# Kernel tuning notes

Measured on AMD Instinct MI355X. Metric: run time of the kernel, lower is better.

## Reference

```python
import jax, jax.numpy as jnp
import numpy as np

EPS = 1e-12

def l2norm(v, axis):
    return v / jnp.maximum(jnp.linalg.norm(v, axis=axis, keepdims=True), EPS)

def setup_inputs() -> dict:
    key = jax.random.key(0)
    k1, k2, k3, k4 = jax.random.split(key, 4)
    N, C, S, K = 16, 128, 16384, 64
    return {
        "x": jax.random.normal(k1, (N, C, S), dtype=jnp.float32),
        "fc_w": jax.random.normal(k2, (K, C), dtype=jnp.float32),
        "fc_b": jax.random.normal(k3, (K,), dtype=jnp.float32),
        "centroids": jax.random.uniform(k4, (K, C), dtype=jnp.float32),
    }

def reference(x, fc_w, fc_b, centroids):
    # x: [N, C, S]; fc_w: [K, C]; centroids: [K, C]
    x = l2norm(x, axis=1)  # descriptor-wise L2 normalize over channels
    # 1x1 conv (per-position linear) -> soft assignment over clusters
    logits = jnp.einsum('ncs,kc->nks', x, fc_w) + fc_b[None, :, None]
    soft = jax.nn.softmax(logits, axis=1)  # [N, K, S]
    # vlad[n,k,c] = sum_s soft[n,k,s] * (x[n,c,s] - centroids[k,c])
    # matmul decomposition avoids materializing [N,K,C,S]
    a_sum = soft.sum(axis=-1)  # [N, K]
    vlad = jnp.einsum('nks,ncs->nkc', soft, x) - a_sum[:, :, None] * centroids[None]
    vlad = l2norm(vlad, axis=2)            # intra-normalization
    vlad = vlad.reshape(vlad.shape[0], -1)  # [N, K*C]
    vlad = l2norm(vlad, axis=1)            # final L2 normalize
    return vlad
```

## Files before the change

### kernel.cpp

```cpp
#include <hip/hip_runtime.h>
#include <hip/hip_fp16.h>

#define N_ 16
#define C_ 128
#define S_ 16384
#define K_ 64

typedef __attribute__((ext_vector_type(4))) float f32x4;
typedef __attribute__((ext_vector_type(8))) _Float16 f16x8;
typedef __attribute__((ext_vector_type(4))) _Float16 f16x4;

#define SWZ_S(s) ((((s) ^ ((s) >> 3)) & 7) << 3)

__global__ __launch_bounds__(256, 2) void fused_kernel(
    const float* __restrict__ x, const float* __restrict__ fc_w,
    const float* __restrict__ fc_b, float* __restrict__ vlad_part,
    float* __restrict__ a_part)
{
    __shared__ _Float16 xT[64 * 128];
    __shared__ _Float16 xC[2][128 * 64];
    __shared__ _Float16 sst[64 * 64];
    __shared__ float rns[2][64];

    const int tid = threadIdx.x;
    const int n = blockIdx.x >> 5;
    const int chunk = blockIdx.x & 31;
    const int lane = tid & 63, w = tid >> 6;
    const int lr = lane & 15, g = lane >> 4;
    const int fsw = (lr & 7) << 3;

    f16x8 wfrag[4][4];
#pragma unroll
    for (int nt = 0; nt < 4; ++nt)
#pragma unroll
        for (int kt = 0; kt < 4; ++kt) {
            const float* wp = fc_w + (nt * 16 + lr) * C_ + kt * 32 + g * 8;
            float4 wa = *(const float4*)wp;
            float4 wb = *(const float4*)(wp + 4);
            f16x8 f;
            f[0] = (_Float16)wa.x; f[1] = (_Float16)wa.y;
            f[2] = (_Float16)wa.z; f[3] = (_Float16)wa.w;
            f[4] = (_Float16)wb.x; f[5] = (_Float16)wb.y;
            f[6] = (_Float16)wb.z; f[7] = (_Float16)wb.w;
            wfrag[nt][kt] = f;
        }
    if (tid < 128) (&rns[0][0])[tid] = 0.f;

    float bias[4];
#pragma unroll
    for (int nt = 0; nt < 4; ++nt) bias[nt] = fc_b[nt * 16 + lr];
    float a_acc[4] = {0.f, 0.f, 0.f, 0.f};
    f32x4 vacc[8];
#pragma unroll
    for (int nt = 0; nt < 8; ++nt) vacc[nt] = (f32x4){0.f, 0.f, 0.f, 0.f};
    f32x4 accp[4];

    const float* xb = x + (size_t)n * C_ * S_;
    const int s4 = tid & 15;
    int cqv[2];
#pragma unroll
    for (int i = 0; i < 2; ++i) cqv[i] = i * 16 + (tid >> 4);

    float4 pre[2][4];
#pragma unroll
    for (int i = 0; i < 2; ++i)
#pragma unroll
        for (int cc = 0; cc < 4; ++cc)
            pre[i][cc] = *(const float4*)(xb + (size_t)(cqv[i] * 4 + cc) * S_ +
                                          chunk * 512 + s4 * 4);

    auto softmax_emit = [&](int pit) {
        float rnl[4], ai[4];
#pragma unroll
        for (int r = 0; r < 4; ++r)
            rnl[r] = 1.0f / fmaxf(sqrtf(rns[pit][w * 16 + g * 4 + r]), 1e-12f);
        if (lane < 16) rns[pit][w * 16 + lane] = 0.f;
#pragma unroll
        for (int nt = 0; nt < 4; ++nt)
#pragma unroll
            for (int r = 0; r < 4; ++r)
                accp[nt][r] = __expf(accp[nt][r] * rnl[r] + bias[nt]);
#pragma unroll
        for (int r = 0; r < 4; ++r) {
            float sum = (accp[0][r] + accp[1][r]) + (accp[2][r] + accp[3][r]);
            sum += __shfl_xor(sum, 1);
            sum += __shfl_xor(sum, 2);
            sum += __shfl_xor(sum, 4);
            sum += __shfl_xor(sum, 8);
            float bi = 1.0f / sum;
            ai[r] = bi * rnl[r];
#pragma unroll
            for (int nt = 0; nt < 4; ++nt) a_acc[nt] += accp[nt][r] * bi;
        }
#pragma unroll
        for (int nt = 0; nt < 4; ++nt) {
            int k = nt * 16 + lr;
            int sloc = w * 16 + g * 4;
            f16x4 p = {(_Float16)(accp[nt][0] * ai[0]), (_Float16)(accp[nt][1] * ai[1]),
                       (_Float16)(accp[nt][2] * ai[2]), (_Float16)(accp[nt][3] * ai[3])};
            *(f16x4*)&sst[k * 64 + (sloc ^ ((k & 7) << 3))] = p;
        }
    };

#pragma unroll 1
    for (int it = 0; it < 8; ++it) {
        const int b = it & 1;
        __syncthreads();

        float part[4] = {0.f, 0.f, 0.f, 0.f};
#pragma unroll
        for (int i = 0; i < 2; ++i) {
            int cq = cqv[i];
#pragma unroll
            for (int jj = 0; jj < 4; ++jj) {
                float v0 = (&pre[i][0].x)[jj], v1 = (&pre[i][1].x)[jj],
                      v2 = (&pre[i][2].x)[jj], v3 = (&pre[i][3].x)[jj];
                part[jj] += v0 * v0 + v1 * v1 + v2 * v2 + v3 * v3;
                f16x4 p = {(_Float16)v0, (_Float16)v1, (_Float16)v2, (_Float16)v3};
                int s = s4 * 4 + jj;
                *(f16x4*)&xT[s * 128 + ((cq * 4) ^ SWZ_S(s))] = p;
            }
#pragma unroll
            for (int cc = 0; cc < 4; ++cc) {
                int c = cq * 4 + cc;
                f16x4 q = {(_Float16)pre[i][cc].x, (_Float16)pre[i][cc].y,
                           (_Float16)pre[i][cc].z, (_Float16)pre[i][cc].w};
                *(f16x4*)&xC[b][c * 64 + ((s4 * 4) ^ ((c & 7) << 3))] = q;
            }
        }
#pragma unroll
        for (int jj = 0; jj < 4; ++jj) {
            part[jj] += __shfl_xor(part[jj], 16);
            part[jj] += __shfl_xor(part[jj], 32);
        }
        if (g == 0) {
#pragma unroll
            for (int jj = 0; jj < 4; ++jj)
                atomicAdd(&rns[it & 1][lr * 4 + jj], part[jj]);
        }
        if (it > 0) softmax_emit((it - 1) & 1);
        if (it < 7) {
            const float* xb2 = xb + chunk * 512 + (it + 1) * 64;
#pragma unroll
            for (int i = 0; i < 2; ++i)
#pragma unroll
                for (int cc = 0; cc < 4; ++cc)
                    pre[i][cc] = *(const float4*)(xb2 + (size_t)(cqv[i] * 4 + cc) * S_ + s4 * 4);
        }
        __syncthreads();

#pragma unroll
        for (int nt = 0; nt < 4; ++nt) accp[nt] = (f32x4){0.f, 0.f, 0.f, 0.f};
        __builtin_amdgcn_s_setprio(1);
#pragma unroll
        for (int kt = 0; kt < 4; ++kt) {
            const int co = kt * 32 + g * 8;
            const int sa = w * 16 + lr;
            f16x8 af = *(const f16x8*)&xT[sa * 128 + (co ^ SWZ_S(sa))];
#pragma unroll
            for (int nt = 0; nt < 4; ++nt)
                accp[nt] = __builtin_amdgcn_mfma_f32_16x16x32_f16(af, wfrag[nt][kt], accp[nt], 0, 0, 0);
        }
        if (it > 0) {
            const _Float16* xcp = xC[b ^ 1];
#pragma unroll
            for (int kt = 0; kt < 2; ++kt) {
                const int so = kt * 32 + g * 8;
                f16x8 pa = *(const f16x8*)&sst[(w * 16 + lr) * 64 + (so ^ fsw)];
#pragma unroll
                for (int nt = 0; nt < 8; ++nt) {
                    f16x8 xv = *(const f16x8*)&xcp[(nt * 16 + lr) * 64 + (so ^ fsw)];
                    vacc[nt] = __builtin_amdgcn_mfma_f32_16x16x32_f16(pa, xv, vacc[nt], 0, 0, 0);
                }
            }
        }
        __builtin_amdgcn_s_setprio(0);
    }

    __syncthreads();
    softmax_emit(1);
    __syncthreads();
    {
        const _Float16* xcp = xC[1];
#pragma unroll
        for (int kt = 0; kt < 2; ++kt) {
            const int so = kt * 32 + g * 8;
            f16x8 pa = *(const f16x8*)&sst[(w * 16 + lr) * 64 + (so ^ fsw)];
#pragma unroll
            for (int nt = 0; nt < 8; ++nt) {
                f16x8 xv = *(const f16x8*)&xcp[(nt * 16 + lr) * 64 + (so ^ fsw)];
                vacc[nt] = __builtin_amdgcn_mfma_f32_16x16x32_f16(pa, xv, vacc[nt], 0, 0, 0);
            }
        }
    }

    float* vp = vlad_part + (size_t)blockIdx.x * (K_ * C_) + (w * 16) * C_;
#pragma unroll
    for (int nt = 0; nt < 8; ++nt)
#pragma unroll
        for (int r = 0; r < 4; ++r)
            vp[(g * 4 + r) * C_ + nt * 16 + lr] = vacc[nt][r];
#pragma unroll
    for (int nt = 0; nt < 4; ++nt) {
        a_acc[nt] += __shfl_xor(a_acc[nt], 16);
        a_acc[nt] += __shfl_xor(a_acc[nt], 32);
    }
    if (lane < 16) {
#pragma unroll
        for (int nt = 0; nt < 4; ++nt)
            a_part[blockIdx.x * 256 + w * 64 + nt * 16 + lr] = a_acc[nt];
    }
}

__global__ __launch_bounds__(256) void reduce_kernel(
    const float* __restrict__ vlad_part, float* __restrict__ vlad_sum)
{
    const int n = blockIdx.x >> 5, g8 = blockIdx.x & 31;
    const int e = g8 * 256 + threadIdx.x;
    const float* p = vlad_part + (size_t)(n * 32) * (K_ * C_) + e;
    float acc = 0.f;
#pragma unroll
    for (int ch = 0; ch < 32; ++ch) acc += p[(size_t)ch * (K_ * C_)];
    vlad_sum[n * (K_ * C_) + e] = acc;
}

__global__ __launch_bounds__(1024) void finalize_kernel(
    const float* __restrict__ vlad_sum, const float* __restrict__ a_part,
    const float* __restrict__ centroids, float* __restrict__ out)
{
    __shared__ float red[16];
    const int n = blockIdx.x;
    const int t = threadIdx.x;
    const int k = t >> 4, q = t & 15;

    float av = 0.f;
#pragma unroll
    for (int cc = 0; cc < 2; ++cc) {
        int ch = q * 2 + cc;
        const float* ap = a_part + (size_t)(n * 32 + ch) * 256 + k;
#pragma unroll
        for (int ww = 0; ww < 4; ++ww) av += ap[ww * 64];
    }
    av += __shfl_xor(av, 1);
    av += __shfl_xor(av, 2);
    av += __shfl_xor(av, 4);
    av += __shfl_xor(av, 8);

    const float* vp = vlad_sum + (size_t)n * (K_ * C_) + k * C_;
    const float* cp = centroids + k * C_;
    float v[8];
    float ssq = 0.f;
#pragma unroll
    for (int jj = 0; jj < 8; ++jj) {
        int c = q + 16 * jj;
        float val = vp[c] - av * cp[c];
        v[jj] = val;
        ssq += val * val;
    }
    ssq += __shfl_xor(ssq, 1);
    ssq += __shfl_xor(ssq, 2);
    ssq += __shfl_xor(ssq, 4);
    ssq += __shfl_xor(ssq, 8);
    const float inv1 = 1.0f / fmaxf(sqrtf(ssq), 1e-12f);

    float gp = (q == 0) ? ssq * inv1 * inv1 : 0.f;
#pragma unroll
    for (int off = 1; off < 64; off <<= 1) gp += __shfl_xor(gp, off);
    if ((t & 63) == 0) red[t >> 6] = gp;
    __syncthreads();
    float G = 0.f;
#pragma unroll
    for (int i = 0; i < 16; ++i) G += red[i];
    const float ginv = 1.0f / fmaxf(sqrtf(G), 1e-12f);

    float* op = out + (size_t)n * (K_ * C_) + k * C_;
#pragma unroll
    for (int jj = 0; jj < 8; ++jj) op[q + 16 * jj] = v[jj] * inv1 * ginv;
}

extern "C" void kernel_launch(void* const* d_in, const int* in_sizes, int n_in,
                              void* d_out, int out_size, void* d_ws, size_t ws_size,
                              hipStream_t stream) {
    const float* x     = (const float*)d_in[0];
    const float* fc_w  = (const float*)d_in[1];
    const float* fc_b  = (const float*)d_in[2];
    const float* cent  = (const float*)d_in[3];
    float* out = (float*)d_out;

    char* ws = (char*)d_ws;
    float* vlad_part = (float*)ws;
    float* a_part    = (float*)(ws + (size_t)512 * K_ * C_ * 4);
    float* vlad_sum  = (float*)(ws + (size_t)512 * K_ * C_ * 4 + 512 * 1024);

    fused_kernel<<<N_ * 32, 256, 0, stream>>>(x, fc_w, fc_b, vlad_part, a_part);
    reduce_kernel<<<N_ * 32, 256, 0, stream>>>(vlad_part, vlad_sum);
    finalize_kernel<<<N_, 1024, 0, stream>>>(vlad_sum, a_part, cent, out);
}
```

Before: 53.85 us.

## Use FP8 MFMA for VLAD aggregation and rebalance grid to 48 chunks per batch

The soft-assignment and x tiles used for the VLAD aggregation matmul are now stored in LDS as FP8, and that matmul runs on fp8×fp8 MFMA. The soft weights are scaled by 256 to keep them in FP8 range, and the scale is undone on output. The grid grows from 512 to 768 blocks, 48 per batch, each handling 5 or 6 tiles of 64 positions, so work spreads more evenly across CUs. This halves LDS traffic for that stage and raises occupancy, at the cost of FP8 accuracy loss, a larger partial buffer, and more partials to reduce.

New measurement: 65.83 us. 22.2% more time.

```diff
diff --git a/kernel.cpp b/kernel.cpp
--- a/kernel.cpp
+++ b/kernel.cpp
@@ -11,6 +11,14 @@
 typedef __attribute__((ext_vector_type(4))) _Float16 f16x4;
 
 #define SWZ_S(s) ((((s) ^ ((s) >> 3)) & 7) << 3)
+#define SWZ8(r) (((r) & 7) << 3)
+
+static __device__ __forceinline__ unsigned int pack_fp8x4(float a, float b,
+                                                          float c, float d) {
+    int v = __builtin_amdgcn_cvt_pk_fp8_f32(a, b, 0, false);
+    v = __builtin_amdgcn_cvt_pk_fp8_f32(c, d, v, true);
+    return (unsigned int)v;
+}
 
 __global__ __launch_bounds__(256, 2) void fused_kernel(
     const float* __restrict__ x, const float* __restrict__ fc_w,
@@ -18,16 +26,19 @@
     float* __restrict__ a_part)
 {
     __shared__ _Float16 xT[64 * 128];
-    __shared__ _Float16 xC[2][128 * 64];
-    __shared__ _Float16 sst[64 * 64];
+    __shared__ __align__(16) unsigned char xC8[2][128 * 64];
+    __shared__ __align__(16) unsigned char sst8[64 * 64];
     __shared__ float rns[2][64];
 
     const int tid = threadIdx.x;
-    const int n = blockIdx.x >> 5;
-    const int chunk = blockIdx.x & 31;
     const int lane = tid & 63, w = tid >> 6;
     const int lr = lane & 15, g = lane >> 4;
-    const int fsw = (lr & 7) << 3;
+    const int fsw = SWZ8(lr);
+
+    const int b = blockIdx.x;
+    const int n = b / 48, j = b % 48;
+    const int lo  = (j < 16) ? j * 6 : 96 + (j - 16) * 5;
+    const int cnt = (j < 16) ? 6 : 5;
 
     f16x8 wfrag[4][4];
 #pragma unroll
@@ -67,7 +78,7 @@
 #pragma unroll
         for (int cc = 0; cc < 4; ++cc)
             pre[i][cc] = *(const float4*)(xb + (size_t)(cqv[i] * 4 + cc) * S_ +
-                                          chunk * 512 + s4 * 4);
+                                          lo * 64 + s4 * 4);
 
     auto softmax_emit = [&](int pit) {
         float rnl[4], ai[4];
@@ -88,7 +99,7 @@
             sum += __shfl_xor(sum, 4);
             sum += __shfl_xor(sum, 8);
             float bi = 1.0f / sum;
-            ai[r] = bi * rnl[r];
+            ai[r] = bi * rnl[r] * 256.0f;
 #pragma unroll
             for (int nt = 0; nt < 4; ++nt) a_acc[nt] += accp[nt][r] * bi;
         }
@@ -96,15 +107,15 @@
         for (int nt = 0; nt < 4; ++nt) {
             int k = nt * 16 + lr;
             int sloc = w * 16 + g * 4;
-            f16x4 p = {(_Float16)(accp[nt][0] * ai[0]), (_Float16)(accp[nt][1] * ai[1]),
-                       (_Float16)(accp[nt][2] * ai[2]), (_Float16)(accp[nt][3] * ai[3])};
-            *(f16x4*)&sst[k * 64 + (sloc ^ ((k & 7) << 3))] = p;
+            unsigned int pk = pack_fp8x4(accp[nt][0] * ai[0], accp[nt][1] * ai[1],
+                                         accp[nt][2] * ai[2], accp[nt][3] * ai[3]);
+            *(unsigned int*)&sst8[k * 64 + (sloc ^ SWZ8(k))] = pk;
         }
     };
 
 #pragma unroll 1
-    for (int it = 0; it < 8; ++it) {
-        const int b = it & 1;
+    for (int it = 0; it < cnt; ++it) {
+        const int bb = it & 1;
         __syncthreads();
 
         float part[4] = {0.f, 0.f, 0.f, 0.f};
@@ -123,9 +134,9 @@
 #pragma unroll
             for (int cc = 0; cc < 4; ++cc) {
                 int c = cq * 4 + cc;
-                f16x4 q = {(_Float16)pre[i][cc].x, (_Float16)pre[i][cc].y,
-                           (_Float16)pre[i][cc].z, (_Float16)pre[i][cc].w};
-                *(f16x4*)&xC[b][c * 64 + ((s4 * 4) ^ ((c & 7) << 3))] = q;
+                unsigned int pk = pack_fp8x4(pre[i][cc].x, pre[i][cc].y,
+                                             pre[i][cc].z, pre[i][cc].w);
+                *(unsigned int*)&xC8[bb][c * 64 + ((s4 * 4) ^ SWZ8(c))] = pk;
             }
         }
 #pragma unroll
@@ -139,8 +150,8 @@
                 atomicAdd(&rns[it & 1][lr * 4 + jj], part[jj]);
         }
         if (it > 0) softmax_emit((it - 1) & 1);
-        if (it < 7) {
-            const float* xb2 = xb + chunk * 512 + (it + 1) * 64;
+        if (it + 1 < cnt) {
+            const float* xb2 = xb + (lo + it + 1) * 64;
 #pragma unroll
             for (int i = 0; i < 2; ++i)
 #pragma unroll
@@ -162,44 +173,45 @@
                 accp[nt] = __builtin_amdgcn_mfma_f32_16x16x32_f16(af, wfrag[nt][kt], accp[nt], 0, 0, 0);
         }
         if (it > 0) {
-            const _Float16* xcp = xC[b ^ 1];
+            const unsigned char* xcp = xC8[bb ^ 1];
 #pragma unroll
             for (int kt = 0; kt < 2; ++kt) {
                 const int so = kt * 32 + g * 8;
-                f16x8 pa = *(const f16x8*)&sst[(w * 16 + lr) * 64 + (so ^ fsw)];
+                long pa = *(const long*)&sst8[(w * 16 + lr) * 64 + (so ^ fsw)];
 #pragma unroll
                 for (int nt = 0; nt < 8; ++nt) {
-                    f16x8 xv = *(const f16x8*)&xcp[(nt * 16 + lr) * 64 + (so ^ fsw)];
-                    vacc[nt] = __builtin_amdgcn_mfma_f32_16x16x32_f16(pa, xv, vacc[nt], 0, 0, 0);
+                    long xv = *(const long*)&xcp[(nt * 16 + lr) * 64 + (so ^ fsw)];
+                    vacc[nt] = __builtin_amdgcn_mfma_f32_16x16x32_fp8_fp8(pa, xv, vacc[nt], 0, 0, 0);
                 }
             }
         }
         __builtin_amdgcn_s_setprio(0);
     }
 
+    const int lastb = (cnt - 1) & 1;
     __syncthreads();
-    softmax_emit(1);
+    softmax_emit(lastb);
     __syncthreads();
     {
-        const _Float16* xcp = xC[1];
+        const unsigned char* xcp = xC8[lastb];
 #pragma unroll
         for (int kt = 0; kt < 2; ++kt) {
             const int so = kt * 32 + g * 8;
-            f16x8 pa = *(const f16x8*)&sst[(w * 16 + lr) * 64 + (so ^ fsw)];
+            long pa = *(const long*)&sst8[(w * 16 + lr) * 64 + (so ^ fsw)];
 #pragma unroll
             for (int nt = 0; nt < 8; ++nt) {
-                f16x8 xv = *(const f16x8*)&xcp[(nt * 16 + lr) * 64 + (so ^ fsw)];
-                vacc[nt] = __builtin_amdgcn_mfma_f32_16x16x32_f16(pa, xv, vacc[nt], 0, 0, 0);
+                long xv = *(const long*)&xcp[(nt * 16 + lr) * 64 + (so ^ fsw)];
+                vacc[nt] = __builtin_amdgcn_mfma_f32_16x16x32_fp8_fp8(pa, xv, vacc[nt], 0, 0, 0);
             }
         }
     }
 
-    float* vp = vlad_part + (size_t)blockIdx.x * (K_ * C_) + (w * 16) * C_;
+    float* vp = vlad_part + (size_t)b * (K_ * C_) + (w * 16) * C_;
 #pragma unroll
     for (int nt = 0; nt < 8; ++nt)
 #pragma unroll
         for (int r = 0; r < 4; ++r)
-            vp[(g * 4 + r) * C_ + nt * 16 + lr] = vacc[nt][r];
+            vp[(g * 4 + r) * C_ + nt * 16 + lr] = vacc[nt][r] * (1.0f / 256.0f);
 #pragma unroll
     for (int nt = 0; nt < 4; ++nt) {
         a_acc[nt] += __shfl_xor(a_acc[nt], 16);
@@ -208,7 +220,7 @@
     if (lane < 16) {
 #pragma unroll
         for (int nt = 0; nt < 4; ++nt)
-            a_part[blockIdx.x * 256 + w * 64 + nt * 16 + lr] = a_acc[nt];
+            a_part[b * 256 + w * 64 + nt * 16 + lr] = a_acc[nt];
     }
 }
 
@@ -217,10 +229,10 @@
 {
     const int n = blockIdx.x >> 5, g8 = blockIdx.x & 31;
     const int e = g8 * 256 + threadIdx.x;
-    const float* p = vlad_part + (size_t)(n * 32) * (K_ * C_) + e;
+    const float* p = vlad_part + (size_t)(n * 48) * (K_ * C_) + e;
     float acc = 0.f;
 #pragma unroll
-    for (int ch = 0; ch < 32; ++ch) acc += p[(size_t)ch * (K_ * C_)];
+    for (int jj = 0; jj < 48; ++jj) acc += p[(size_t)jj * (K_ * C_)];
     vlad_sum[n * (K_ * C_) + e] = acc;
 }
 
@@ -235,9 +247,9 @@
 
     float av = 0.f;
 #pragma unroll
-    for (int cc = 0; cc < 2; ++cc) {
-        int ch = q * 2 + cc;
-        const float* ap = a_part + (size_t)(n * 32 + ch) * 256 + k;
+    for (int cc = 0; cc < 3; ++cc) {
+        int ch = q * 3 + cc;
+        const float* ap = a_part + (size_t)(n * 48 + ch) * 256 + k;
 #pragma unroll
         for (int ww = 0; ww < 4; ++ww) av += ap[ww * 64];
     }
@@ -289,10 +301,10 @@
 
     char* ws = (char*)d_ws;
     float* vlad_part = (float*)ws;
-    float* a_part    = (float*)(ws + (size_t)512 * K_ * C_ * 4);
-    float* vlad_sum  = (float*)(ws + (size_t)512 * K_ * C_ * 4 + 512 * 1024);
-
-    fused_kernel<<<N_ * 32, 256, 0, stream>>>(x, fc_w, fc_b, vlad_part, a_part);
-    reduce_kernel<<<N_ * 32, 256, 0, stream>>>(vlad_part, vlad_sum);
+    float* a_part    = (float*)(ws + (size_t)768 * K_ * C_ * 4);
+    float* vlad_sum  = (float*)(ws + (size_t)768 * K_ * C_ * 4 + 786432);
+
+    fused_kernel<<<768, 256, 0, stream>>>(x, fc_w, fc_b, vlad_part, a_part);
+    reduce_kernel<<<512, 256, 0, stream>>>(vlad_part, vlad_sum);
     finalize_kernel<<<N_, 1024, 0, stream>>>(vlad_sum, a_part, cent, out);
 }
```
